# Kernel tuning notes

Measured on AMD Instinct MI355X. Metric: run time of the kernel, lower is better.

The kernel has to match this reference:

```python
import jax, jax.numpy as jnp
import numpy as np

B, T, C = 4, 2048, 1024
NH = 16
HD = C // NH


def setup_inputs() -> dict:
    key = jax.random.key(0)
    k1, k2, k3 = jax.random.split(key, 3)
    x = jax.random.normal(k1, (B, T, C), dtype=jnp.float32)
    Wqkv = jax.random.normal(k2, (C, 3 * C), dtype=jnp.float32) * 0.02
    bqkv = jnp.zeros((3 * C,), dtype=jnp.float32)
    Wproj = jax.random.normal(k3, (C, C), dtype=jnp.float32) * 0.02
    bproj = jnp.zeros((C,), dtype=jnp.float32)
    return {"x": x, "Wqkv": Wqkv, "bqkv": bqkv, "Wproj": Wproj, "bproj": bproj}


def reference(x, Wqkv, bqkv, Wproj, bproj):
    Bx, Tx, Cx = x.shape
    qkv = x @ Wqkv + bqkv  # [B,T,3C]
    q, k, v = jnp.split(qkv, 3, axis=-1)
    # [B, NH, T, HD]
    q = q.reshape(Bx, Tx, NH, HD).transpose(0, 2, 1, 3)
    k = k.reshape(Bx, Tx, NH, HD).transpose(0, 2, 1, 3)
    v = v.reshape(Bx, Tx, NH, HD).transpose(0, 2, 1, 3)
    scale = 1.0 / jnp.sqrt(jnp.float32(HD))
    att = jnp.einsum('bhqd,bhkd->bhqk', q, k) * scale  # [B,NH,T,T]
    causal = jnp.tril(jnp.ones((Tx, Tx), dtype=bool))
    att = jnp.where(causal, att, jnp.float32(-jnp.inf))
    att = jax.nn.softmax(att, axis=-1)
    y = jnp.einsum('bhqk,bhkd->bhqd', att, v)  # [B,NH,T,HD]
    y = y.transpose(0, 2, 1, 3).reshape(Bx, Tx, Cx)
    return y @ Wproj + bproj
```

## Files before the change

kernel.cpp:

```cpp
#include <hip/hip_runtime.h>
#include <hip/hip_bf16.h>
#include <math.h>

#define B_  4
#define T_  2048
#define C_  1024
#define NH_ 16
#define HD_ 64

using bf16 = __hip_bfloat16;
typedef __attribute__((ext_vector_type(8))) short bf16x8;
typedef __attribute__((ext_vector_type(4))) short bf16x4;
typedef __attribute__((ext_vector_type(4))) float f32x4;

__device__ __forceinline__ bf16 f2b(float f){ return __float2bfloat16(f); }

__device__ __forceinline__ short f2bs(float f){
  union { float f; unsigned u; } x; x.f = f;
  x.u += 0x7FFFu + ((x.u >> 16) & 1u);
  return (short)(x.u >> 16);
}

__device__ __forceinline__ bf16x4 pack_bf16x4(float a, float b, float c, float d){
  union { bf16x4 v; __hip_bfloat162 h[2]; } u;
  u.h[0] = __float22bfloat162_rn(make_float2(a, b));
  u.h[1] = __float22bfloat162_rn(make_float2(c, d));
  return u.v;
}

__device__ __forceinline__ float fexp2(float x){
  float r; asm("v_exp_f32 %0, %1" : "=v"(r) : "v"(x)); return r;
}

__device__ __forceinline__ void async_load16(const bf16* g, bf16* l){
  __builtin_amdgcn_global_load_lds((const __attribute__((address_space(1))) unsigned int*)g,
                                   (__attribute__((address_space(3))) unsigned int*)l,
                                   16, 0, 0);
}

#define QSCALE 0.18033688011112042f

__global__ __launch_bounds__(256) void k_prep(const float* __restrict__ x, bf16* __restrict__ xb, int n,
                                              const float* __restrict__ in0, bf16* __restrict__ out0,
                                              const float* __restrict__ in1, bf16* __restrict__ out1){
  __shared__ float t[32][33];
  int b = blockIdx.x;
  if (b < 8192){
    int i = (b * 256 + threadIdx.x) * 4;
    if (i < n){
      float4 f = *(const float4*)(x + i);
      ushort4 u;
      u.x = (unsigned short)f2bs(f.x);
      u.y = (unsigned short)f2bs(f.y);
      u.z = (unsigned short)f2bs(f.z);
      u.w = (unsigned short)f2bs(f.w);
      *(ushort4*)(xb + i) = u;
    }
    return;
  }
  b -= 8192;
  const float* in; bf16* out; int Cc, bx, by;
  if (b < 3072){ in = in0; out = out0; Cc = 3*C_; bx = (b % 96)*32; by = (b / 96)*32; }
  else { b -= 3072; in = in1; out = out1; Cc = C_; bx = (b & 31)*32; by = (b >> 5)*32; }
  const int R = C_;
  int lx = threadIdx.x & 31, ly = threadIdx.x >> 5;
  #pragma unroll
  for (int s = 0; s < 4; s++){
    int k = by + ly + s*8;
    t[ly + s*8][lx] = in[(size_t)k * Cc + bx + lx];
  }
  __syncthreads();
  #pragma unroll
  for (int s = 0; s < 4; s++){
    int n2 = bx + ly + s*8;
    out[(size_t)n2 * R + by + lx] = f2b(t[lx][ly + s*8]);
  }
}

template<int MODE>
__global__ __launch_bounds__(256, 2) void k_gemm8(
    const bf16* __restrict__ A, const bf16* __restrict__ BT,
    const float* __restrict__ bias,
    bf16* __restrict__ qo, bf16* __restrict__ ko, bf16* __restrict__ vo,
    float* __restrict__ fout,
    int M, int N, int K)
{
  __shared__ bf16 As[2][2][128*32];
  __shared__ bf16 Bs[2][2][128*32];

  const int tid  = threadIdx.x;
  const int wave = tid >> 6, lane = tid & 63;
  const int wm = wave & 1, wn = wave >> 1;
  const int quad = lane >> 4, l15 = lane & 15;
  const int bm = blockIdx.x * 128;
  const int bn = blockIdx.y * 128;

  const bf16* gA[2]; const bf16* gB[2]; int lofs[2];
  #pragma unroll
  for (int s = 0; s < 2; s++){
    const int c = tid + s*256;
    const int r = c >> 2, p = (c & 3) ^ ((r >> 1) & 3);
    gA[s] = A  + (size_t)(bm + r)*K + p*8;
    gB[s] = BT + (size_t)(bn + r)*K + p*8;
    lofs[s] = c*8;
  }
  const int fsw = (l15 >> 1) & 3;

  f32x4 acc[4][4] = {};
  const int nT = K >> 6;

  #pragma unroll
  for (int kh = 0; kh < 2; kh++)
    #pragma unroll
    for (int s = 0; s < 2; s++){
      async_load16(gA[s] + kh*32, &As[0][kh][0] + lofs[s]);
      async_load16(gB[s] + kh*32, &Bs[0][kh][0] + lofs[s]);
    }

  for (int u = 0; u < nT; u++){
    const int d = u & 1;
    #pragma unroll
    for (int kh = 0; kh < 2; kh++){
      if (u + 1 < nT || kh == 0) asm volatile("s_waitcnt vmcnt(4)" ::: "memory");
      else                       asm volatile("s_waitcnt vmcnt(0)" ::: "memory");
      __builtin_amdgcn_s_barrier();
      __builtin_amdgcn_sched_barrier(0);

      const bf16* as = &As[d][kh][0];
      const bf16* bs = &Bs[d][kh][0];
      bf16x8 af[4], bfv[4];
      #pragma unroll
      for (int i = 0; i < 4; i++)
        af[i]  = *reinterpret_cast<const bf16x8*>(as + (wm*64 + i*16 + l15)*32 + ((quad ^ fsw) << 3));
      #pragma unroll
      for (int j = 0; j < 4; j++)
        bfv[j] = *reinterpret_cast<const bf16x8*>(bs + (wn*64 + j*16 + l15)*32 + ((quad ^ fsw) << 3));

      if (u + 1 < nT){
        const int ko2 = (u + 1)*64 + kh*32;
        #pragma unroll
        for (int s = 0; s < 2; s++){
          async_load16(gA[s] + ko2, &As[d^1][kh][0] + lofs[s]);
          async_load16(gB[s] + ko2, &Bs[d^1][kh][0] + lofs[s]);
        }
      }

      __builtin_amdgcn_s_setprio(1);
      #pragma unroll
      for (int i = 0; i < 4; i++)
        #pragma unroll
        for (int j = 0; j < 4; j++)
          acc[i][j] = __builtin_amdgcn_mfma_f32_16x16x32_bf16(af[i], bfv[j], acc[i][j], 0, 0, 0);
      __builtin_amdgcn_s_setprio(0);
    }
  }

  if (MODE == 0){
    const int sec = bn >> 10;
    const int bb2 = bm >> 11;
    const int tb  = (bm & (T_ - 1)) + wm*64 + quad*4;
    const int hn  = ((bn & 1023) >> 6) + wn;
    const size_t bhx = (size_t)(bb2 * NH_ + hn);
    if (sec == 2){
      #pragma unroll
      for (int j = 0; j < 4; j++){
        const int d2 = j*16 + l15;
        const float bj = bias[bn + wn*64 + j*16 + l15];
        bf16* vrow = vo + (bhx * HD_ + d2) * (size_t)T_;
        const int sw = (l15 & 7) * 8;
        #pragma unroll
        for (int i = 0; i < 4; i++){
          const int t = (tb + i*16) ^ sw;
          *reinterpret_cast<bf16x4*>(vrow + t) =
            pack_bf16x4(acc[i][j][0] + bj, acc[i][j][1] + bj,
                        acc[i][j][2] + bj, acc[i][j][3] + bj);
        }
      }
    } else {
      bf16* dst = (sec == 0) ? qo : ko;
      const float sc = (sec == 0) ? QSCALE : 1.0f;
      bf16* base = dst + bhx * T_ * HD_;
      float bj[4];
      #pragma unroll
      for (int j = 0; j < 4; j++) bj[j] = bias[bn + wn*64 + j*16 + l15];
      #pragma unroll
      for (int i = 0; i < 4; i++){
        #pragma unroll
        for (int r = 0; r < 4; r++){
          const int t  = tb + i*16 + r;
          const int sw2 = (t & 7) * 8;
          bf16* prow = base + (size_t)t * HD_;
          #pragma unroll
          for (int j = 0; j < 4; j++){
            const int dq = (j*16 + l15) ^ sw2;
            short s = f2bs((acc[i][j][r] + bj[j]) * sc);
            prow[dq] = *(bf16*)&s;
          }
        }
      }
    }
  } else {
    const int n0 = bn + wn*64 + l15;
    float bj[4];
    #pragma unroll
    for (int j = 0; j < 4; j++) bj[j] = bias[n0 + j*16];
    #pragma unroll
    for (int i = 0; i < 4; i++){
      #pragma unroll
      for (int r = 0; r < 4; r++){
        float* p0 = fout + (size_t)(bm + wm*64 + i*16 + quad*4 + r) * N + n0;
        #pragma unroll
        for (int j = 0; j < 4; j++)
          p0[j*16] = acc[i][j][r] + bj[j];
      }
    }
  }
}

__global__ __launch_bounds__(256) void k_attn(
    const bf16* __restrict__ Q, const bf16* __restrict__ Kg,
    const bf16* __restrict__ Vt, bf16* __restrict__ Y)
{
  __shared__ bf16 Ks[2][64*64];
  __shared__ bf16 Vs[2][64*64];

  const int bh = blockIdx.x;
  const int bb = bh >> 4, hh = bh & 15;
  const int qt = 15 - blockIdx.y;
  const int tid  = threadIdx.x;
  const int wave = tid >> 6, lane = tid & 63;
  const int quad = lane >> 4, l15 = lane & 15;
  const int swz  = (l15 & 7) * 8;

  const size_t baseQK = (size_t)bh * T_ * HD_;
  const size_t baseV  = (size_t)bh * HD_ * T_;

  const int ca = wave, cb = wave + 4;
  const bf16* kg_a = Kg + baseQK + ca*512 + (size_t)lane*8;
  const bf16* kg_b = Kg + baseQK + cb*512 + (size_t)lane*8;
  const bf16* vg_a = Vt + baseV + (size_t)(ca*8 + (lane>>3)) * T_ + (lane&7)*8;
  const bf16* vg_b = Vt + baseV + (size_t)(cb*8 + (lane>>3)) * T_ + (lane&7)*8;
  bf16* kl_a0 = &Ks[0][0] + ca*512;  bf16* kl_b0 = &Ks[0][0] + cb*512;
  bf16* vl_a0 = &Vs[0][0] + ca*512;  bf16* vl_b0 = &Vs[0][0] + cb*512;

  bf16x4 ones_f;
  {
    short v = (l15 == 0) ? f2bs(1.0f) : (short)0;
    ones_f = (bf16x4){ v, v, v, v };
  }
  const f32x4 ZV = {0.0f, 0.0f, 0.0f, 0.0f};

  const int jmax = 2*qt + 1;

  bf16x8 qf[2][2];
  #pragma unroll
  for (int s = 0; s < 2; s++){
    const int t = qt*128 + s*64 + wave*16 + l15;
    #pragma unroll
    for (int ks = 0; ks < 2; ks++){
      const int col = (ks*32 + quad*8) ^ swz;
      qf[s][ks] = *reinterpret_cast<const bf16x8*>(Q + baseQK + (size_t)t*HD_ + col);
    }
  }

  async_load16(kg_a, kl_a0);  async_load16(kg_b, kl_b0);
  async_load16(vg_a, vl_a0);  async_load16(vg_b, vl_b0);

  f32x4 o[2][5] = {};

  for (int j = 0; j <= jmax; j++){
    __syncthreads();

    if (j < jmax){
      const int nb = ((j+1) & 1) * 4096;
      const size_t ko = (size_t)(j+1) * 64 * HD_;
      async_load16(kg_a + ko, kl_a0 + nb);  async_load16(kg_b + ko, kl_b0 + nb);
      async_load16(vg_a + (j+1)*64, vl_a0 + nb);
      async_load16(vg_b + (j+1)*64, vl_b0 + nb);
    }

    const bf16* ksb = &Ks[j & 1][0];
    const bf16* vsb = &Vs[j & 1][0];

    f32x4 st[2][4];
    __builtin_amdgcn_s_setprio(1);
    #pragma unroll
    for (int tk = 0; tk < 4; tk++){
      bf16x8 kf0 = *reinterpret_cast<const bf16x8*>(ksb + (tk*16 + l15)*64 + ((quad*8) ^ swz));
      bf16x8 kf1 = *reinterpret_cast<const bf16x8*>(ksb + (tk*16 + l15)*64 + ((32 + quad*8) ^ swz));
      st[0][tk] = __builtin_amdgcn_mfma_f32_16x16x32_bf16(kf0, qf[0][0], ZV, 0, 0, 0);
      st[1][tk] = __builtin_amdgcn_mfma_f32_16x16x32_bf16(kf0, qf[1][0], ZV, 0, 0, 0);
      st[0][tk] = __builtin_amdgcn_mfma_f32_16x16x32_bf16(kf1, qf[0][1], st[0][tk], 0, 0, 0);
      st[1][tk] = __builtin_amdgcn_mfma_f32_16x16x32_bf16(kf1, qf[1][1], st[1][tk], 0, 0, 0);
    }
    __builtin_amdgcn_s_setprio(0);

    bf16x4 pf[2][4];
    #pragma unroll
    for (int s = 0; s < 2; s++){
      const int qg = qt*128 + s*64 + wave*16 + l15;
      const bool msk = s ? (j > 2*qt) : (j >= 2*qt);
      #pragma unroll
      for (int tk = 0; tk < 4; tk++){
        float e[4];
        #pragma unroll
        for (int r = 0; r < 4; r++){
          float sv = st[s][tk][r];
          if (msk){
            const int kvg = j*64 + tk*16 + quad*4 + r;
            if (kvg > qg) sv = -1e30f;
          }
          e[r] = fexp2(sv);
        }
        pf[s][tk] = pack_bf16x4(e[0], e[1], e[2], e[3]);
      }
    }

    __builtin_amdgcn_s_setprio(1);
    #pragma unroll
    for (int td = 0; td < 4; td++){
      #pragma unroll
      for (int tk = 0; tk < 4; tk++){
        bf16x4 vf = *reinterpret_cast<const bf16x4*>(vsb + (td*16 + l15)*64 + ((tk*16 + quad*4) ^ swz));
        o[0][td] = __builtin_amdgcn_mfma_f32_16x16x16bf16_1k(vf, pf[0][tk], o[0][td], 0, 0, 0);
        o[1][td] = __builtin_amdgcn_mfma_f32_16x16x16bf16_1k(vf, pf[1][tk], o[1][td], 0, 0, 0);
      }
    }
    #pragma unroll
    for (int tk = 0; tk < 4; tk++){
      o[0][4] = __builtin_amdgcn_mfma_f32_16x16x16bf16_1k(ones_f, pf[0][tk], o[0][4], 0, 0, 0);
      o[1][4] = __builtin_amdgcn_mfma_f32_16x16x16bf16_1k(ones_f, pf[1][tk], o[1][4], 0, 0, 0);
    }
    __builtin_amdgcn_s_setprio(0);
  }

  #pragma unroll
  for (int s = 0; s < 2; s++){
    const float l = __shfl(o[s][4][0], l15, 64);
    const float inv = 1.0f / l;
    const int t = qt*128 + s*64 + wave*16 + l15;
    bf16* yrow = Y + ((size_t)(bb * T_ + t)) * C_ + hh * HD_;
    #pragma unroll
    for (int td = 0; td < 4; td++){
      *reinterpret_cast<bf16x4*>(yrow + td*16 + quad*4) =
        pack_bf16x4(o[s][td][0] * inv, o[s][td][1] * inv,
                    o[s][td][2] * inv, o[s][td][3] * inv);
    }
  }
}


extern "C" void kernel_launch(void* const* d_in, const int* in_sizes, int n_in,
                              void* d_out, int out_size, void* d_ws, size_t ws_size,
                              hipStream_t stream) {
  const float* x     = (const float*)d_in[0];
  const float* Wqkv  = (const float*)d_in[1];
  const float* bqkv  = (const float*)d_in[2];
  const float* Wproj = (const float*)d_in[3];
  const float* bproj = (const float*)d_in[4];
  float* out = (float*)d_out;

  const size_t M = (size_t)B_ * T_;
  char* w = (char*)d_ws;
  bf16* xb     = (bf16*)w;  w += M * C_ * 2;
  bf16* WqkvT  = (bf16*)w;  w += (size_t)3 * C_ * C_ * 2;
  bf16* WprojT = (bf16*)w;  w += (size_t)C_ * C_ * 2;
  bf16* Qb     = (bf16*)w;  w += M * C_ * 2;
  bf16* Kb     = (bf16*)w;  w += M * C_ * 2;
  bf16* Vtb    = (bf16*)w;  w += M * C_ * 2;
  bf16* Yb     = (bf16*)w;  w += M * C_ * 2;

  {
    int n = (int)(M * C_);
    k_prep<<<dim3(12288), dim3(256), 0, stream>>>(x, xb, n, Wqkv, WqkvT, Wproj, WprojT);
  }
  k_gemm8<0><<<dim3(M/128, (3*C_)/128), dim3(256), 0, stream>>>(
      xb, WqkvT, bqkv, Qb, Kb, Vtb, nullptr, (int)M, 3*C_, C_);
  k_attn<<<dim3(64, 16), dim3(256), 0, stream>>>(Qb, Kb, Vtb, Yb);
  k_gemm8<1><<<dim3(M/128, C_/128), dim3(256), 0, stream>>>(
      Yb, WprojT, bproj, nullptr, nullptr, nullptr, out, (int)M, C_, C_);
}
```

Baseline: 236.7 us.

## Replace double-buffered GEMM K pipeline with three-slot ring buffer

Rewrites the GEMM main loop so it steps through K in 32-wide slices using a 3-slot LDS ring buffer with a prefetch distance of two slices, instead of double buffering 64-wide tiles split into halves. This cuts shared memory per block from four slices to three, which may allow higher occupancy and simplifies loop control. The min-blocks hint is dropped from launch bounds, so the compiler may now use more registers per thread. The 3-slot ring relies on the per-step barrier to keep a slot from being overwritten while other waves may still be reading it.

```diff
diff --git a/kernel.cpp b/kernel.cpp
--- a/kernel.cpp
+++ b/kernel.cpp
@@ -78,15 +78,15 @@
 }
 
 template<int MODE>
-__global__ __launch_bounds__(256, 2) void k_gemm8(
+__global__ __launch_bounds__(256) void k_gemm9(
     const bf16* __restrict__ A, const bf16* __restrict__ BT,
     const float* __restrict__ bias,
     bf16* __restrict__ qo, bf16* __restrict__ ko, bf16* __restrict__ vo,
     float* __restrict__ fout,
     int M, int N, int K)
 {
-  __shared__ bf16 As[2][2][128*32];
-  __shared__ bf16 Bs[2][2][128*32];
+  __shared__ bf16 As[3][128*32];
+  __shared__ bf16 Bs[3][128*32];
 
   const int tid  = threadIdx.x;
   const int wave = tid >> 6, lane = tid & 63;
@@ -107,52 +107,52 @@
   const int fsw = (l15 >> 1) & 3;
 
   f32x4 acc[4][4] = {};
-  const int nT = K >> 6;
-
-  #pragma unroll
-  for (int kh = 0; kh < 2; kh++)
+  const int S = K >> 5;
+
+  #pragma unroll
+  for (int t = 0; t < 2; t++)
     #pragma unroll
     for (int s = 0; s < 2; s++){
-      async_load16(gA[s] + kh*32, &As[0][kh][0] + lofs[s]);
-      async_load16(gB[s] + kh*32, &Bs[0][kh][0] + lofs[s]);
-    }
-
-  for (int u = 0; u < nT; u++){
-    const int d = u & 1;
-    #pragma unroll
-    for (int kh = 0; kh < 2; kh++){
-      if (u + 1 < nT || kh == 0) asm volatile("s_waitcnt vmcnt(4)" ::: "memory");
-      else                       asm volatile("s_waitcnt vmcnt(0)" ::: "memory");
-      __builtin_amdgcn_s_barrier();
-      __builtin_amdgcn_sched_barrier(0);
-
-      const bf16* as = &As[d][kh][0];
-      const bf16* bs = &Bs[d][kh][0];
-      bf16x8 af[4], bfv[4];
-      #pragma unroll
-      for (int i = 0; i < 4; i++)
-        af[i]  = *reinterpret_cast<const bf16x8*>(as + (wm*64 + i*16 + l15)*32 + ((quad ^ fsw) << 3));
+      async_load16(gA[s] + t*32, &As[t][0] + lofs[s]);
+      async_load16(gB[s] + t*32, &Bs[t][0] + lofs[s]);
+    }
+
+  int slot = 0, sslot = 2;
+  for (int t = 0; t < S; t++){
+    if (t < S - 1) asm volatile("s_waitcnt vmcnt(4)" ::: "memory");
+    else           asm volatile("s_waitcnt vmcnt(0)" ::: "memory");
+    __builtin_amdgcn_s_barrier();
+    __builtin_amdgcn_sched_barrier(0);
+
+    const bf16* as = &As[slot][0];
+    const bf16* bs = &Bs[slot][0];
+    bf16x8 af[4], bfv[4];
+    #pragma unroll
+    for (int i = 0; i < 4; i++)
+      af[i]  = *reinterpret_cast<const bf16x8*>(as + (wm*64 + i*16 + l15)*32 + ((quad ^ fsw) << 3));
+    #pragma unroll
+    for (int j = 0; j < 4; j++)
+      bfv[j] = *reinterpret_cast<const bf16x8*>(bs + (wn*64 + j*16 + l15)*32 + ((quad ^ fsw) << 3));
+
+    if (t + 2 < S){
+      const int ko2 = (t + 2) * 32;
+      #pragma unroll
+      for (int s = 0; s < 2; s++){
+        async_load16(gA[s] + ko2, &As[sslot][0] + lofs[s]);
+        async_load16(gB[s] + ko2, &Bs[sslot][0] + lofs[s]);
+      }
+    }
+
+    __builtin_amdgcn_s_setprio(1);
+    #pragma unroll
+    for (int i = 0; i < 4; i++)
       #pragma unroll
       for (int j = 0; j < 4; j++)
-        bfv[j] = *reinterpret_cast<const bf16x8*>(bs + (wn*64 + j*16 + l15)*32 + ((quad ^ fsw) << 3));
-
-      if (u + 1 < nT){
-        const int ko2 = (u + 1)*64 + kh*32;
-        #pragma unroll
-        for (int s = 0; s < 2; s++){
-          async_load16(gA[s] + ko2, &As[d^1][kh][0] + lofs[s]);
-          async_load16(gB[s] + ko2, &Bs[d^1][kh][0] + lofs[s]);
-        }
-      }
-
-      __builtin_amdgcn_s_setprio(1);
-      #pragma unroll
-      for (int i = 0; i < 4; i++)
-        #pragma unroll
-        for (int j = 0; j < 4; j++)
-          acc[i][j] = __builtin_amdgcn_mfma_f32_16x16x32_bf16(af[i], bfv[j], acc[i][j], 0, 0, 0);
-      __builtin_amdgcn_s_setprio(0);
-    }
+        acc[i][j] = __builtin_amdgcn_mfma_f32_16x16x32_bf16(af[i], bfv[j], acc[i][j], 0, 0, 0);
+    __builtin_amdgcn_s_setprio(0);
+
+    slot  = (slot  == 2) ? 0 : slot  + 1;
+    sslot = (sslot == 2) ? 0 : sslot + 1;
   }
 
   if (MODE == 0){
@@ -374,9 +374,9 @@
     int n = (int)(M * C_);
     k_prep<<<dim3(12288), dim3(256), 0, stream>>>(x, xb, n, Wqkv, WqkvT, Wproj, WprojT);
   }
-  k_gemm8<0><<<dim3(M/128, (3*C_)/128), dim3(256), 0, stream>>>(
+  k_gemm9<0><<<dim3(M/128, (3*C_)/128), dim3(256), 0, stream>>>(
       xb, WqkvT, bqkv, Qb, Kb, Vtb, nullptr, (int)M, 3*C_, C_);
   k_attn<<<dim3(64, 16), dim3(256), 0, stream>>>(Qb, Kb, Vtb, Yb);
-  k_gemm8<1><<<dim3(M/128, C_/128), dim3(256), 0, stream>>>(
+  k_gemm9<1><<<dim3(M/128, C_/128), dim3(256), 0, stream>>>(
       Yb, WprojT, bproj, nullptr, nullptr, nullptr, out, (int)M, C_, C_);
 }
```

Measured after the change: 237.8 us. No clear change (+0.5%).

## Peel last causal KV tile in attention and widen weight transpose tiles

Applied to the files above, without the earlier changes.

The attention loop now runs the interior tiles without the s=1 masking branch and peels the final diagonal KV tile. In that peeled tile only the second 64-row query half computes QK^T, softmax and PV, which skips the MFMA work the first half would have spent on fully masked entries. The weight transpose in k_prep now handles 64-row tiles and writes packed bf16 pairs, halving the transpose blocks and widening its stores. The cost is larger code and more LDS per prep block.

```diff
diff --git a/kernel.cpp b/kernel.cpp
--- a/kernel.cpp
+++ b/kernel.cpp
@@ -43,7 +43,7 @@
 __global__ __launch_bounds__(256) void k_prep(const float* __restrict__ x, bf16* __restrict__ xb, int n,
                                               const float* __restrict__ in0, bf16* __restrict__ out0,
                                               const float* __restrict__ in1, bf16* __restrict__ out1){
-  __shared__ float t[32][33];
+  __shared__ float t[64][33];
   int b = blockIdx.x;
   if (b < 8192){
     int i = (b * 256 + threadIdx.x) * 4;
@@ -60,20 +60,24 @@
   }
   b -= 8192;
   const float* in; bf16* out; int Cc, bx, by;
-  if (b < 3072){ in = in0; out = out0; Cc = 3*C_; bx = (b % 96)*32; by = (b / 96)*32; }
-  else { b -= 3072; in = in1; out = out1; Cc = C_; bx = (b & 31)*32; by = (b >> 5)*32; }
+  if (b < 1536){ in = in0; out = out0; Cc = 3*C_; bx = (b % 96)*32; by = (b / 96)*64; }
+  else { b -= 1536; in = in1; out = out1; Cc = C_; bx = (b & 31)*32; by = (b >> 5)*64; }
   const int R = C_;
   int lx = threadIdx.x & 31, ly = threadIdx.x >> 5;
   #pragma unroll
-  for (int s = 0; s < 4; s++){
+  for (int s = 0; s < 8; s++){
     int k = by + ly + s*8;
     t[ly + s*8][lx] = in[(size_t)k * Cc + bx + lx];
   }
   __syncthreads();
   #pragma unroll
   for (int s = 0; s < 4; s++){
-    int n2 = bx + ly + s*8;
-    out[(size_t)n2 * R + by + lx] = f2b(t[lx][ly + s*8]);
+    const int nl = ly + s*8;
+    const int n2 = bx + nl;
+    ushort2 v;
+    v.x = (unsigned short)f2bs(t[2*lx    ][nl]);
+    v.y = (unsigned short)f2bs(t[2*lx + 1][nl]);
+    *(ushort2*)(out + (size_t)n2 * R + by + 2*lx) = v;
   }
 }
 
@@ -250,8 +254,6 @@
   }
   const f32x4 ZV = {0.0f, 0.0f, 0.0f, 0.0f};
 
-  const int jmax = 2*qt + 1;
-
   bf16x8 qf[2][2];
   #pragma unroll
   for (int s = 0; s < 2; s++){
@@ -268,10 +270,10 @@
 
   f32x4 o[2][5] = {};
 
-  for (int j = 0; j <= jmax; j++){
+  for (int j = 0; j <= 2*qt; j++){
     __syncthreads();
 
-    if (j < jmax){
+    {
       const int nb = ((j+1) & 1) * 4096;
       const size_t ko = (size_t)(j+1) * 64 * HD_;
       async_load16(kg_a + ko, kl_a0 + nb);  async_load16(kg_b + ko, kl_b0 + nb);
@@ -296,24 +298,30 @@
     __builtin_amdgcn_s_setprio(0);
 
     bf16x4 pf[2][4];
-    #pragma unroll
-    for (int s = 0; s < 2; s++){
-      const int qg = qt*128 + s*64 + wave*16 + l15;
-      const bool msk = s ? (j > 2*qt) : (j >= 2*qt);
+    {
+      const int qg = qt*128 + wave*16 + l15;
+      const bool msk = (j == 2*qt);
       #pragma unroll
       for (int tk = 0; tk < 4; tk++){
         float e[4];
         #pragma unroll
         for (int r = 0; r < 4; r++){
-          float sv = st[s][tk][r];
+          float sv = st[0][tk][r];
           if (msk){
             const int kvg = j*64 + tk*16 + quad*4 + r;
             if (kvg > qg) sv = -1e30f;
           }
           e[r] = fexp2(sv);
         }
-        pf[s][tk] = pack_bf16x4(e[0], e[1], e[2], e[3]);
-      }
+        pf[0][tk] = pack_bf16x4(e[0], e[1], e[2], e[3]);
+      }
+    }
+    #pragma unroll
+    for (int tk = 0; tk < 4; tk++){
+      float e[4];
+      #pragma unroll
+      for (int r = 0; r < 4; r++) e[r] = fexp2(st[1][tk][r]);
+      pf[1][tk] = pack_bf16x4(e[0], e[1], e[2], e[3]);
     }
 
     __builtin_amdgcn_s_setprio(1);
@@ -331,6 +339,56 @@
       o[0][4] = __builtin_amdgcn_mfma_f32_16x16x16bf16_1k(ones_f, pf[0][tk], o[0][4], 0, 0, 0);
       o[1][4] = __builtin_amdgcn_mfma_f32_16x16x16bf16_1k(ones_f, pf[1][tk], o[1][4], 0, 0, 0);
     }
+    __builtin_amdgcn_s_setprio(0);
+  }
+
+  {
+    const int j = 2*qt + 1;
+    __syncthreads();
+
+    const bf16* ksb = &Ks[j & 1][0];
+    const bf16* vsb = &Vs[j & 1][0];
+
+    f32x4 st1[4];
+    __builtin_amdgcn_s_setprio(1);
+    #pragma unroll
+    for (int tk = 0; tk < 4; tk++){
+      bf16x8 kf0 = *reinterpret_cast<const bf16x8*>(ksb + (tk*16 + l15)*64 + ((quad*8) ^ swz));
+      bf16x8 kf1 = *reinterpret_cast<const bf16x8*>(ksb + (tk*16 + l15)*64 + ((32 + quad*8) ^ swz));
+      st1[tk] = __builtin_amdgcn_mfma_f32_16x16x32_bf16(kf0, qf[1][0], ZV, 0, 0, 0);
+      st1[tk] = __builtin_amdgcn_mfma_f32_16x16x32_bf16(kf1, qf[1][1], st1[tk], 0, 0, 0);
+    }
+    __builtin_amdgcn_s_setprio(0);
+
+    bf16x4 pf1[4];
+    {
+      const int qg = qt*128 + 64 + wave*16 + l15;
+      #pragma unroll
+      for (int tk = 0; tk < 4; tk++){
+        float e[4];
+        #pragma unroll
+        for (int r = 0; r < 4; r++){
+          float sv = st1[tk][r];
+          const int kvg = j*64 + tk*16 + quad*4 + r;
+          if (kvg > qg) sv = -1e30f;
+          e[r] = fexp2(sv);
+        }
+        pf1[tk] = pack_bf16x4(e[0], e[1], e[2], e[3]);
+      }
+    }
+
+    __builtin_amdgcn_s_setprio(1);
+    #pragma unroll
+    for (int td = 0; td < 4; td++){
+      #pragma unroll
+      for (int tk = 0; tk < 4; tk++){
+        bf16x4 vf = *reinterpret_cast<const bf16x4*>(vsb + (td*16 + l15)*64 + ((tk*16 + quad*4) ^ swz));
+        o[1][td] = __builtin_amdgcn_mfma_f32_16x16x16bf16_1k(vf, pf1[tk], o[1][td], 0, 0, 0);
+      }
+    }
+    #pragma unroll
+    for (int tk = 0; tk < 4; tk++)
+      o[1][4] = __builtin_amdgcn_mfma_f32_16x16x16bf16_1k(ones_f, pf1[tk], o[1][4], 0, 0, 0);
     __builtin_amdgcn_s_setprio(0);
   }
 
@@ -372,7 +430,7 @@
 
   {
     int n = (int)(M * C_);
-    k_prep<<<dim3(12288), dim3(256), 0, stream>>>(x, xb, n, Wqkv, WqkvT, Wproj, WprojT);
+    k_prep<<<dim3(10240), dim3(256), 0, stream>>>(x, xb, n, Wqkv, WqkvT, Wproj, WprojT);
   }
   k_gemm8<0><<<dim3(M/128, (3*C_)/128), dim3(256), 0, stream>>>(
       xb, WqkvT, bqkv, Qb, Kb, Vtb, nullptr, (int)M, 3*C_, C_);
```

Measured after the change: 238.7 us. About the same (+0.9%).
